# Performance work log

Hardware: AMD Instinct MI355X
Metric: run time of the kernel (lower is better)

The kernel has to match this reference:

```python
import jax, jax.numpy as jnp
import numpy as np

B = 4
CPD = 64            # control_plane_dim
RES = 64            # n_resonances
N_SAMPLES = 131072
CONTROL_RATE = 256
N_FRAMES = N_SAMPLES // CONTROL_RATE  # 512
FILTER_SIZE = 2048
HID = 16            # hypernetwork hidden
BASE_RESONANCE = 0.5
MAX_RESONANCE = 0.9999


def _sequential_damping(forces, damping):
    # forces, damping: (b, cpd, T); out[0]=f[0]; out[i]=(f[i]+out[i-1])*d[i]
    f_t = jnp.moveaxis(forces, -1, 0)   # (T, b, cpd)
    d_t = jnp.moveaxis(damping, -1, 0)  # (T, b, cpd)
    first = jnp.zeros((f_t.shape[0],), dtype=bool).at[0].set(True)

    def step(carry, xs):
        f, d, fst = xs
        out = jnp.where(fst, f, (f + carry) * d)
        return out, out

    _, ys = jax.lax.scan(step, jnp.zeros_like(f_t[0]), (f_t, d_t, first))
    return jnp.moveaxis(ys, 0, -1)


def _interp_linear(x, out_size):
    # F.interpolate(mode='linear', align_corners=False) along last axis
    n = x.shape[-1]
    pos = (jnp.arange(out_size, dtype=jnp.float32) + 0.5) * (n / out_size) - 0.5
    pos = jnp.clip(pos, 0.0, n - 1)
    i0 = jnp.floor(pos).astype(jnp.int32)
    i1 = jnp.minimum(i0 + 1, n - 1)
    frac = (pos - i0).astype(x.dtype)
    return x[..., i0] * (1.0 - frac) + x[..., i1] * frac


def _fft_convolve(a, b):
    # pad both to 2N, multiply spectra, keep first N (linear convolution)
    n = a.shape[-1]
    pa = jnp.pad(a, [(0, 0)] * (a.ndim - 1) + [(0, n)])
    pb = jnp.pad(b, [(0, 0)] * (b.ndim - 1) + [(0, n)])
    spec = jnp.fft.rfft(pa, axis=-1) * jnp.fft.rfft(pb, axis=-1)
    return jnp.fft.irfft(spec, axis=-1)[..., :n]


def setup_inputs() -> dict:
    key = jax.random.key(0)
    ks = jax.random.split(key, 9)
    forces = jax.random.normal(ks[0], (B, CPD, N_FRAMES), jnp.float32) * 0.1
    damping_modifier = jax.random.normal(ks[1], (B, CPD, N_FRAMES), jnp.float32) * 0.001
    noise = jax.random.uniform(ks[2], (B, RES, N_SAMPLES), jnp.float32, -0.01, 0.01)
    damping_param = jnp.zeros((1, CPD, 1), jnp.float32)
    routing = jax.random.uniform(ks[3], (1, 1, CPD, RES), jnp.float32, -0.01, 0.01)
    W1 = jax.random.normal(ks[4], (CPD, HID), jnp.float32) / jnp.sqrt(jnp.float32(CPD))
    b1 = jnp.zeros((HID,), jnp.float32)
    W2 = jax.random.normal(ks[5], (HID, CPD * RES), jnp.float32) / jnp.sqrt(jnp.float32(HID))
    b2 = jnp.zeros((CPD * RES,), jnp.float32)
    filters = jax.random.uniform(ks[6], (1, RES, FILTER_SIZE), jnp.float32, -0.01, 0.01)
    to_control = jax.random.uniform(ks[7], (RES, CPD), jnp.float32, -0.01, 0.01)
    return dict(forces=forces, damping_modifier=damping_modifier, noise=noise,
                damping_param=damping_param, routing=routing,
                W1=W1, b1=b1, W2=W2, b2=b2,
                filters=filters, to_control=to_control)


def reference(forces, damping_modifier, noise, damping_param, routing,
              W1, b1, W2, b2, filters, to_control):
    batch = forces.shape[0]
    # Damping module
    damping = BASE_RESONANCE + jax.nn.sigmoid(damping_param) * (MAX_RESONANCE - BASE_RESONANCE)
    damping = jnp.broadcast_to(damping, (1, CPD, N_FRAMES))
    damping = jnp.clip(damping - jnp.abs(damping_modifier), 0.0, 1.0)  # (b,cpd,T)
    damped = _sequential_damping(forces, damping)                       # (b,cpd,T)

    # HyperNetworkLayer: per-frame routing weight modifier
    x = jnp.swapaxes(damped, 1, 2)                      # (b, T, cpd)
    h = jax.nn.leaky_relu(x @ W1 + b1, negative_slope=0.2)
    w = (h @ W2 + b2).reshape(batch, N_FRAMES, CPD, RES)
    w = w + routing                                      # (b, T, cpd, res)

    routed = jnp.einsum('abc,acbd->adc', damped, w)      # (b, res, T)
    to_ctrl = jnp.einsum('brf,rc->bcf', routed, to_control)  # (b, cpd, T)

    upsampled = _interp_linear(routed, N_SAMPLES)        # (b, res, N)
    energy = upsampled * noise
    filt = jnp.pad(filters, ((0, 0), (0, 0), (0, N_SAMPLES - FILTER_SIZE)))
    with_resonance = _fft_convolve(energy, filt)         # (b, res, N)
    return to_ctrl, with_resonance
```

## Files before the change

kernel.cpp:

```cpp
#include <hip/hip_runtime.h>
#include <cstdint>

#define BATCH 4
#define CPD 64
#define RES 64
#define NS 131072
#define NF 512
#define FS 2048
#define HID 16

typedef _Float16 __attribute__((ext_vector_type(8))) f16x8;
typedef float __attribute__((ext_vector_type(16))) f32x16;

__global__ __launch_bounds__(256) void k_scan(const float* __restrict__ forces,
                                              const float* __restrict__ dmod,
                                              const float* __restrict__ dparam,
                                              float* __restrict__ damped_t) {
  __shared__ float f_lds[64][129];
  __shared__ float d_lds[64][129];
  const int b = blockIdx.x;
  const int tid = threadIdx.x;
  float dbase = 0.f, carry = 0.f;
  if (tid < 64) {
    float dp = dparam[tid];
    dbase = 0.5f + (0.9999f - 0.5f) / (1.f + expf(-dp));
  }
  for (int ch = 0; ch < 4; ++ch) {
    const int t0 = ch * 128;
    __syncthreads();
    for (int idx = tid; idx < 64 * 128; idx += 256) {
      int c = idx >> 7, tl = idx & 127;
      f_lds[c][tl] = forces[(b * CPD + c) * NF + t0 + tl];
      d_lds[c][tl] = dmod[(b * CPD + c) * NF + t0 + tl];
    }
    __syncthreads();
    if (tid < 64) {
      const int c = tid;
      for (int tl = 0; tl < 128; ++tl) {
        float d = dbase - fabsf(d_lds[c][tl]);
        d = fminf(fmaxf(d, 0.f), 1.f);
        float f = f_lds[c][tl];
        float out = (ch == 0 && tl == 0) ? f : (f + carry) * d;
        carry = out;
        damped_t[(b * NF + t0 + tl) * CPD + c] = out;
      }
    }
  }
}

__global__ __launch_bounds__(256) void k_hyper(const float* __restrict__ damped_t,
                                               const float* __restrict__ routing,
                                               const float* __restrict__ W1,
                                               const float* __restrict__ b1,
                                               const float* __restrict__ W2,
                                               const float* __restrict__ b2,
                                               const float* __restrict__ to_control,
                                               float* __restrict__ routed,
                                               float* __restrict__ to_ctrl) {
  __shared__ float xs[4][64];
  __shared__ float hs[4][16];
  __shared__ float rs[4][64];
  const int blk = blockIdx.x;
  const int b = blk >> 7;
  const int t0 = (blk & 127) * 4;
  const int lt = threadIdx.x >> 6;
  const int d = threadIdx.x & 63;
  const int t = t0 + lt;

  xs[lt][d] = damped_t[(b * NF + t) * CPD + d];
  __syncthreads();
  if (d < HID) {
    float a = b1[d];
    for (int c = 0; c < CPD; ++c) a = fmaf(xs[lt][c], W1[c * HID + d], a);
    hs[lt][d] = a > 0.f ? a : 0.2f * a;
  }
  __syncthreads();
  float hreg[HID];
#pragma unroll
  for (int j = 0; j < HID; ++j) hreg[j] = hs[lt][j];

  float acc = 0.f;
  for (int c = 0; c < CPD; ++c) {
    float w = routing[c * RES + d] + b2[c * RES + d];
    const float* w2p = W2 + c * RES + d;
#pragma unroll
    for (int j = 0; j < HID; ++j) w = fmaf(hreg[j], w2p[j * (CPD * RES)], w);
    acc = fmaf(xs[lt][c], w, acc);
  }
  routed[(b * RES + d) * NF + t] = acc;
  rs[lt][d] = acc;
  __syncthreads();
  float tc = 0.f;
  for (int q = 0; q < RES; ++q) tc = fmaf(rs[lt][q], to_control[q * CPD + d], tc);
  to_ctrl[(b * CPD + d) * NF + t] = tc;
}

#define ER_N 34832
#define ER_G 4360
#define FCP_DW 1072

__global__ __launch_bounds__(512, 4) void k_conv(const float* __restrict__ routed,
                                                 const float* __restrict__ noise,
                                                 const float* __restrict__ filters,
                                                 float* __restrict__ outp) {
  __shared__ __align__(16) unsigned short er[ER_G * 8];
  __shared__ __align__(16) unsigned fcp[2 * FCP_DW];

  const int tid = threadIdx.x;
  const int seg = blockIdx.x & 3;
  const int r = (blockIdx.x >> 2) & 63;
  const int b = blockIdx.x >> 8;
  const int NB = seg * 32768;
  const int E0 = NB + 32776;
  const int chan = b * RES + r;
  const float* rp = routed + chan * NF;
  const float* npz = noise + (size_t)chan * NS;

  for (int idx = tid; idx < 2 * FCP_DW; idx += 512) {
    int p = idx >= FCP_DW;
    int q = idx - p * FCP_DW;
    int t0 = 2 * q + p - 40;
    float f0 = (t0 >= 0 && t0 < FS) ? filters[r * FS + t0] : 0.f;
    float f1 = (t0 + 1 >= 0 && t0 + 1 < FS) ? filters[r * FS + t0 + 1] : 0.f;
    union { _Float16 h[2]; unsigned u; } P;
    P.h[0] = (_Float16)f0;
    P.h[1] = (_Float16)f1;
    fcp[idx] = P.u;
  }

  unsigned* er32 = (unsigned*)er;
  for (int x2 = tid; x2 < ER_N / 2; x2 += 512) {
    int x = 2 * x2;
    union { _Float16 h[2]; unsigned u; } P;
#pragma unroll
    for (int k = 0; k < 2; ++k) {
      int n = E0 - x - k;
      float e = 0.f;
      if (n >= 0 && n < NS) {
        float pos = ((float)n + 0.5f) * (1.f / 256.f) - 0.5f;
        pos = fminf(fmaxf(pos, 0.f), 511.f);
        float fi = floorf(pos);
        int i0 = (int)fi;
        int i1 = min(i0 + 1, 511);
        float fr = pos - fi;
        float u = rp[i0] * (1.f - fr) + rp[i1] * fr;
        e = u * npz[n];
      }
      P.h[k] = (_Float16)(e * 1024.f);
    }
    int g = x >> 3;
    int sig = g ^ ((g >> 3) & 7);
    er32[sig * 4 + ((x & 7) >> 1)] = P.u;
  }
  __syncthreads();

  const int w = tid >> 6;
  const int l = tid & 63;
  const int row = l & 31;
  const int h = l >> 5;

  const int gb0 = 4092 - 512 * w - 4 * row + h;
  int qB = (row >> 1) + 4 * h + (row & 1) * FCP_DW;

  f32x16 acc0, acc1, acc2, acc3;
#pragma unroll
  for (int i = 0; i < 16; ++i) { acc0[i] = 0.f; acc1[i] = 0.f; acc2[i] = 0.f; acc3[i] = 0.f; }

  for (int s = 0; s < 131; ++s) {
    union { unsigned u[4]; f16x8 v; } Bf;
    Bf.u[0] = fcp[qB];
    Bf.u[1] = fcp[qB + 1];
    Bf.u[2] = fcp[qB + 2];
    Bf.u[3] = fcp[qB + 3];
    const int s2 = 2 * s;
#define TILE(ACC, GB)                                                         \
    {                                                                         \
      int g = (GB) + s2;                                                      \
      int ab = (g ^ ((g >> 3) & 7)) << 4;                                     \
      union { uint4 u; f16x8 v; } Af;                                         \
      Af.u = *(const uint4*)((const char*)er + ab);                           \
      ACC = __builtin_amdgcn_mfma_f32_32x32x16_f16(Af.v, Bf.v, ACC, 0, 0, 0); \
    }
    TILE(acc0, gb0)
    TILE(acc1, gb0 - 128)
    TILE(acc2, gb0 - 256)
    TILE(acc3, gb0 - 384)
#undef TILE
    qB += 8;
  }

  float* base = outp + (size_t)chan * NS + NB;
#define STORE(ACC, TAU)                                                       \
  {                                                                           \
    float* po = base + 1024 * (4 * w + (TAU));                                \
    _Pragma("unroll")                                                         \
    for (int rg = 0; rg < 16; ++rg) {                                         \
      int crow = (rg & 3) + 8 * (rg >> 2) + 4 * h;                            \
      po[32 * crow + row] = ACC[rg] * (1.f / 1024.f);                         \
    }                                                                         \
  }
  STORE(acc0, 0)
  STORE(acc1, 1)
  STORE(acc2, 2)
  STORE(acc3, 3)
#undef STORE
}

extern "C" void kernel_launch(void* const* d_in, const int* in_sizes, int n_in,
                              void* d_out, int out_size, void* d_ws, size_t ws_size,
                              hipStream_t stream) {
  const float* forces     = (const float*)d_in[0];
  const float* dmod       = (const float*)d_in[1];
  const float* noise      = (const float*)d_in[2];
  const float* dparam     = (const float*)d_in[3];
  const float* routing    = (const float*)d_in[4];
  const float* W1         = (const float*)d_in[5];
  const float* b1         = (const float*)d_in[6];
  const float* W2         = (const float*)d_in[7];
  const float* b2         = (const float*)d_in[8];
  const float* filters    = (const float*)d_in[9];
  const float* to_control = (const float*)d_in[10];

  float* out = (float*)d_out;
  float* to_ctrl = out;
  float* reso = out + BATCH * CPD * NF;

  float* damped_t = (float*)d_ws;
  float* routed = damped_t + BATCH * NF * CPD;

  k_scan<<<BATCH, 256, 0, stream>>>(forces, dmod, dparam, damped_t);
  k_hyper<<<BATCH * NF / 4, 256, 0, stream>>>(damped_t, routing, W1, b1, W2, b2,
                                              to_control, routed, to_ctrl);
  k_conv<<<BATCH * RES * (NS / 32768), 512, 0, stream>>>(routed, noise, filters, reso);
}
```

Baseline: 235.1 us.

## Restructure MFMA convolution to reuse A fragments across two filter halves

The MFMA inner loop now loads each signal fragment once and multiplies it against two filter-tap halves, producing eight accumulators per wave and halving the loop trip count. Partial sums from adjacent waves are combined through shared memory, and segment boundary contributions go to the output with atomic adds. A new zeroing kernel clears the boundary regions first. This raises register pressure (launch bounds occupancy drops from 4 to 2) and adds atomics, an extra launch and a special tail loop for the last segment.

```diff
diff --git a/kernel.cpp b/kernel.cpp
--- a/kernel.cpp
+++ b/kernel.cpp
@@ -95,31 +95,48 @@
   to_ctrl[(b * CPD + d) * NF + t] = tc;
 }
 
-#define ER_N 34832
-#define ER_G 4360
-#define FCP_DW 1072
-
-__global__ __launch_bounds__(512, 4) void k_conv(const float* __restrict__ routed,
+__global__ __launch_bounds__(256) void k_zero(float* __restrict__ reso) {
+  const int chan = blockIdx.x;
+  const size_t base = (size_t)chan * NS;
+  for (int i = threadIdx.x; i < 4096; i += 256) {
+    int y;
+    if (i < 32) y = i;
+    else if (i < 32 + 3072) {
+      int s = 1 + ((i - 32) >> 10);
+      y = 32768 * s - 992 + ((i - 32) & 1023);
+    } else {
+      y = 130080 + (i - 3104);
+    }
+    reso[base + y] = 0.f;
+  }
+}
+
+#define ER_GRAN 4360
+#define ER_N 34816
+#define FQ 1068
+
+__global__ __launch_bounds__(512, 2) void k_conv(const float* __restrict__ routed,
                                                  const float* __restrict__ noise,
                                                  const float* __restrict__ filters,
                                                  float* __restrict__ outp) {
-  __shared__ __align__(16) unsigned short er[ER_G * 8];
-  __shared__ __align__(16) unsigned fcp[2 * FCP_DW];
+  __shared__ __align__(16) unsigned char smem[ER_GRAN * 16 + 2 * FQ * 4];
+  unsigned short* er = (unsigned short*)smem;
+  unsigned* fcp = (unsigned*)(smem + ER_GRAN * 16);
 
   const int tid = threadIdx.x;
   const int seg = blockIdx.x & 3;
   const int r = (blockIdx.x >> 2) & 63;
   const int b = blockIdx.x >> 8;
-  const int NB = seg * 32768;
-  const int E0 = NB + 32776;
+  const int SegB = seg * 32768;
+  const int E0 = SegB + 32800;
   const int chan = b * RES + r;
   const float* rp = routed + chan * NF;
   const float* npz = noise + (size_t)chan * NS;
 
-  for (int idx = tid; idx < 2 * FCP_DW; idx += 512) {
-    int p = idx >= FCP_DW;
-    int q = idx - p * FCP_DW;
-    int t0 = 2 * q + p - 40;
+  for (int idx = tid; idx < 2 * FQ; idx += 512) {
+    int p = idx >= FQ;
+    int q = idx - p * FQ;
+    int t0 = 2 * q + p - 48;
     float f0 = (t0 >= 0 && t0 < FS) ? filters[r * FS + t0] : 0.f;
     float f1 = (t0 + 1 >= 0 && t0 + 1 < FS) ? filters[r * FS + t0 + 1] : 0.f;
     union { _Float16 h[2]; unsigned u; } P;
@@ -128,29 +145,31 @@
     fcp[idx] = P.u;
   }
 
-  unsigned* er32 = (unsigned*)er;
-  for (int x2 = tid; x2 < ER_N / 2; x2 += 512) {
-    int x = 2 * x2;
-    union { _Float16 h[2]; unsigned u; } P;
-#pragma unroll
-    for (int k = 0; k < 2; ++k) {
-      int n = E0 - x - k;
-      float e = 0.f;
-      if (n >= 0 && n < NS) {
-        float pos = ((float)n + 0.5f) * (1.f / 256.f) - 0.5f;
-        pos = fminf(fmaxf(pos, 0.f), 511.f);
-        float fi = floorf(pos);
-        int i0 = (int)fi;
-        int i1 = min(i0 + 1, 511);
-        float fr = pos - fi;
-        float u = rp[i0] * (1.f - fr) + rp[i1] * fr;
-        e = u * npz[n];
+  {
+    unsigned* er32 = (unsigned*)er;
+    for (int x2 = tid; x2 < ER_N / 2; x2 += 512) {
+      int x = 2 * x2;
+      union { _Float16 h[2]; unsigned u; } P;
+#pragma unroll
+      for (int k = 0; k < 2; ++k) {
+        int n = E0 - x - k;
+        float e = 0.f;
+        if (n >= 0 && n < NS) {
+          float pos = ((float)n + 0.5f) * (1.f / 256.f) - 0.5f;
+          pos = fminf(fmaxf(pos, 0.f), 511.f);
+          float fi = floorf(pos);
+          int i0 = (int)fi;
+          int i1 = min(i0 + 1, 511);
+          float fr = pos - fi;
+          float u = rp[i0] * (1.f - fr) + rp[i1] * fr;
+          e = u * npz[n];
+        }
+        P.h[k] = (_Float16)(e * 1024.f);
       }
-      P.h[k] = (_Float16)(e * 1024.f);
-    }
-    int g = x >> 3;
-    int sig = g ^ ((g >> 3) & 7);
-    er32[sig * 4 + ((x & 7) >> 1)] = P.u;
+      int g = x >> 3;
+      int sig = g ^ ((g >> 3) & 7);
+      er32[sig * 4 + ((x & 7) >> 1)] = P.u;
+    }
   }
   __syncthreads();
 
@@ -158,52 +177,118 @@
   const int l = tid & 63;
   const int row = l & 31;
   const int h = l >> 5;
-
-  const int gb0 = 4092 - 512 * w - 4 * row + h;
-  int qB = (row >> 1) + 4 * h + (row & 1) * FCP_DW;
-
-  f32x16 acc0, acc1, acc2, acc3;
-#pragma unroll
-  for (int i = 0; i < 16; ++i) { acc0[i] = 0.f; acc1[i] = 0.f; acc2[i] = 0.f; acc3[i] = 0.f; }
-
-  for (int s = 0; s < 131; ++s) {
-    union { unsigned u[4]; f16x8 v; } Bf;
-    Bf.u[0] = fcp[qB];
-    Bf.u[1] = fcp[qB + 1];
-    Bf.u[2] = fcp[qB + 2];
-    Bf.u[3] = fcp[qB + 3];
-    const int s2 = 2 * s;
-#define TILE(ACC, GB)                                                         \
-    {                                                                         \
-      int g = (GB) + s2;                                                      \
-      int ab = (g ^ ((g >> 3) & 7)) << 4;                                     \
-      union { uint4 u; f16x8 v; } Af;                                         \
-      Af.u = *(const uint4*)((const char*)er + ab);                           \
-      ACC = __builtin_amdgcn_mfma_f32_32x32x16_f16(Af.v, Bf.v, ACC, 0, 0, 0); \
-    }
-    TILE(acc0, gb0)
-    TILE(acc1, gb0 - 128)
-    TILE(acc2, gb0 - 256)
-    TILE(acc3, gb0 - 384)
-#undef TILE
-    qB += 8;
-  }
-
-  float* base = outp + (size_t)chan * NS + NB;
-#define STORE(ACC, TAU)                                                       \
+  const int p = row & 1;
+
+  int ga0 = 4096 - 512 * w + 4 * row + h;
+  int ga1 = ga0 - 128;
+  int ga2 = ga0 - 256;
+  int ga3 = ga0 - 384;
+  int qB = ((row - p) >> 1) + 8 + 4 * h + p * FQ;
+
+  f32x16 a00, a01, a02, a03, a10, a11, a12, a13;
+#pragma unroll
+  for (int i = 0; i < 16; ++i) {
+    a00[i] = 0.f; a01[i] = 0.f; a02[i] = 0.f; a03[i] = 0.f;
+    a10[i] = 0.f; a11[i] = 0.f; a12[i] = 0.f; a13[i] = 0.f;
+  }
+
+#define LOADB(DST, Q)                                                         \
+  union { unsigned u[4]; f16x8 v; } DST;                                      \
+  DST.u[0] = fcp[(Q)]; DST.u[1] = fcp[(Q) + 1];                               \
+  DST.u[2] = fcp[(Q) + 2]; DST.u[3] = fcp[(Q) + 3];
+#define LOADA(DST, G)                                                         \
+  union { uint4 u; f16x8 v; } DST;                                            \
+  { int ab = ((G) ^ (((G) >> 3) & 7)) << 4;                                   \
+    DST.u = *(const uint4*)((const unsigned char*)er + ab); }
+
+  for (int sg = 0; sg < 2; ++sg) {
+    LOADB(Bf, qB)
+    LOADA(A0, ga0) LOADA(A1, ga1) LOADA(A2, ga2) LOADA(A3, ga3)
+    a00 = __builtin_amdgcn_mfma_f32_32x32x16_f16(A0.v, Bf.v, a00, 0, 0, 0);
+    a01 = __builtin_amdgcn_mfma_f32_32x32x16_f16(A1.v, Bf.v, a01, 0, 0, 0);
+    a02 = __builtin_amdgcn_mfma_f32_32x32x16_f16(A2.v, Bf.v, a02, 0, 0, 0);
+    a03 = __builtin_amdgcn_mfma_f32_32x32x16_f16(A3.v, Bf.v, a03, 0, 0, 0);
+    ga0 += 2; ga1 += 2; ga2 += 2; ga3 += 2; qB += 8;
+  }
+  for (int sg = 0; sg < 64; ++sg) {
+    LOADB(B0, qB)
+    LOADB(B1, qB + 512)
+    LOADA(A0, ga0) LOADA(A1, ga1) LOADA(A2, ga2) LOADA(A3, ga3)
+    a00 = __builtin_amdgcn_mfma_f32_32x32x16_f16(A0.v, B0.v, a00, 0, 0, 0);
+    a10 = __builtin_amdgcn_mfma_f32_32x32x16_f16(A0.v, B1.v, a10, 0, 0, 0);
+    a01 = __builtin_amdgcn_mfma_f32_32x32x16_f16(A1.v, B0.v, a01, 0, 0, 0);
+    a11 = __builtin_amdgcn_mfma_f32_32x32x16_f16(A1.v, B1.v, a11, 0, 0, 0);
+    a02 = __builtin_amdgcn_mfma_f32_32x32x16_f16(A2.v, B0.v, a02, 0, 0, 0);
+    a12 = __builtin_amdgcn_mfma_f32_32x32x16_f16(A2.v, B1.v, a12, 0, 0, 0);
+    a03 = __builtin_amdgcn_mfma_f32_32x32x16_f16(A3.v, B0.v, a03, 0, 0, 0);
+    a13 = __builtin_amdgcn_mfma_f32_32x32x16_f16(A3.v, B1.v, a13, 0, 0, 0);
+    ga0 += 2; ga1 += 2; ga2 += 2; ga3 += 2; qB += 8;
+  }
+
+  if (seg == 3 && w == 7) {
+    f32x16 ax;
+#pragma unroll
+    for (int i = 0; i < 16; ++i) ax[i] = 0.f;
+    int ge = 4 * row + h;
+    int qx = ((row - p) >> 1) + 8 + 4 * h + p * FQ;
+    for (int sg = 0; sg < 66; ++sg) {
+      LOADB(Bx, qx)
+      LOADA(Ax, ge)
+      ax = __builtin_amdgcn_mfma_f32_32x32x16_f16(Ax.v, Bx.v, ax, 0, 0, 0);
+      ge += 2; qx += 8;
+    }
+#pragma unroll
+    for (int i = 0; i < 16; ++i) a13[i] += ax[i];
+  }
+#undef LOADA
+#undef LOADB
+
+  float* cbase = outp + (size_t)chan * NS;
+  const float scale = 1.f / 1024.f;
+
+#define SUMSTORE(P0, P1, U)                                                   \
   {                                                                           \
-    float* po = base + 1024 * (4 * w + (TAU));                                \
+    float* po = cbase + SegB + 4096 * w + 1024 * (U);                         \
     _Pragma("unroll")                                                         \
     for (int rg = 0; rg < 16; ++rg) {                                         \
       int crow = (rg & 3) + 8 * (rg >> 2) + 4 * h;                            \
-      po[32 * crow + row] = ACC[rg] * (1.f / 1024.f);                         \
+      po[row - 32 * crow] = (P0[rg] + P1[rg]) * scale;                        \
     }                                                                         \
   }
-  STORE(acc0, 0)
-  STORE(acc1, 1)
-  STORE(acc2, 2)
-  STORE(acc3, 3)
-#undef STORE
+  SUMSTORE(a01, a10, 1)
+  SUMSTORE(a02, a11, 2)
+  SUMSTORE(a03, a12, 3)
+#undef SUMSTORE
+
+  __syncthreads();
+  float* scr = (float*)smem;
+#pragma unroll
+  for (int rg = 0; rg < 16; ++rg) scr[w * 1024 + rg * 64 + l] = a13[rg];
+  __syncthreads();
+
+  if (w >= 1) {
+    float* po = cbase + SegB + 4096 * w;
+#pragma unroll
+    for (int rg = 0; rg < 16; ++rg) {
+      int crow = (rg & 3) + 8 * (rg >> 2) + 4 * h;
+      po[row - 32 * crow] = (a00[rg] + scr[(w - 1) * 1024 + rg * 64 + l]) * scale;
+    }
+  } else {
+#pragma unroll
+    for (int rg = 0; rg < 16; ++rg) {
+      int crow = (rg & 3) + 8 * (rg >> 2) + 4 * h;
+      int y = SegB + row - 32 * crow;
+      if (y >= 0) atomicAdd(cbase + y, a00[rg] * scale);
+    }
+  }
+  if (w == 7) {
+#pragma unroll
+    for (int rg = 0; rg < 16; ++rg) {
+      int crow = (rg & 3) + 8 * (rg >> 2) + 4 * h;
+      int y = SegB + 32768 + row - 32 * crow;
+      if (y < NS) atomicAdd(cbase + y, a13[rg] * scale);
+    }
+  }
 }
 
 extern "C" void kernel_launch(void* const* d_in, const int* in_sizes, int n_in,
@@ -231,5 +316,6 @@
   k_scan<<<BATCH, 256, 0, stream>>>(forces, dmod, dparam, damped_t);
   k_hyper<<<BATCH * NF / 4, 256, 0, stream>>>(damped_t, routing, W1, b1, W2, b2,
                                               to_control, routed, to_ctrl);
+  k_zero<<<BATCH * RES, 256, 0, stream>>>(reso);
   k_conv<<<BATCH * RES * (NS / 32768), 512, 0, stream>>>(routed, noise, filters, reso);
 }
```

New measurement: 268.6 us. 14.3% more time.
